# Performance work log

Hardware: AMD Instinct MI355X
Metric: run time of the kernel (lower is better)

## Reference

```python
import math
import jax, jax.numpy as jnp
import numpy as np

EMBED_DIM = 1024
N_HEADS = 16
HEAD_DIM = EMBED_DIM // N_HEADS
B, T = 4, 2048


def setup_inputs() -> dict:
    key = jax.random.key(0)
    k1, k2, k3 = jax.random.split(key, 3)
    scale_in = 1.0 / math.sqrt(EMBED_DIM)
    return {
        "x": jax.random.normal(k1, (B, T, EMBED_DIM), dtype=jnp.float32),
        "direction": 0,  # 0=FORWARD (causal), 1=RETRODICTION (anti-causal), 2=CORRECTION (causal)
        "qkv_w": jax.random.normal(k2, (EMBED_DIM, 3 * EMBED_DIM), dtype=jnp.float32) * scale_in,
        "qkv_b": jnp.zeros((3 * EMBED_DIM,), dtype=jnp.float32),
        "proj_w": jax.random.normal(k3, (EMBED_DIM, EMBED_DIM), dtype=jnp.float32) * scale_in,
        "proj_b": jnp.zeros((EMBED_DIM,), dtype=jnp.float32),
    }


def reference(x, direction, qkv_w, qkv_b, proj_w, proj_b):
    Bx, Tx, C = x.shape
    qkv = x @ qkv_w + qkv_b                        # [B,T,3C]
    q, k, v = jnp.split(qkv, 3, axis=-1)
    # [B,T,C] -> [B,H,T,D]
    def heads(t):
        return t.reshape(Bx, Tx, N_HEADS, HEAD_DIM).transpose(0, 2, 1, 3)
    q, k, v = heads(q), heads(k), heads(v)
    scale = 1.0 / math.sqrt(HEAD_DIM)
    attn = jnp.einsum('bhqd,bhkd->bhqk', q, k) * scale
    rows = jnp.arange(Tx)[:, None]
    cols = jnp.arange(Tx)[None, :]
    if direction == 1:  # RETRODICTION -> anti-causal (upper triangular allowed)
        mask = cols >= rows
    else:               # FORWARD / CORRECTION -> causal
        mask = cols <= rows
    attn = jnp.where(mask[None, None], attn, -jnp.inf)
    attn = jax.nn.softmax(attn, axis=-1)  # dropout p=0 -> identity
    out = jnp.einsum('bhqk,bhkd->bhqd', attn, v)   # [B,H,T,D]
    out = out.transpose(0, 2, 1, 3).reshape(Bx, Tx, C)
    return out @ proj_w + proj_b
```

## Files before the change

kernel.cpp:

```cpp
#include <hip/hip_runtime.h>
#include <math.h>

typedef __bf16 bf16_t;
typedef bf16_t bf16x8 __attribute__((ext_vector_type(8)));
typedef bf16_t bf16x4 __attribute__((ext_vector_type(4)));
typedef float  f32x4  __attribute__((ext_vector_type(4)));
typedef float  floatv4 __attribute__((ext_vector_type(4)));

#define AS1 __attribute__((address_space(1)))
#define AS3 __attribute__((address_space(3)))

static __device__ __forceinline__ void gld_lds16(const void* g, void* l) {
  __builtin_amdgcn_global_load_lds((const AS1 unsigned int*)g,
                                   (AS3 unsigned int*)l, 16, 0, 0);
}
static __device__ __forceinline__ void block_sync() {
  asm volatile("" ::: "memory");
  __builtin_amdgcn_s_barrier();
  asm volatile("" ::: "memory");
}

__global__ __launch_bounds__(256) void k_cast(const float* __restrict__ in,
                                              bf16_t* __restrict__ out, int n4) {
  int i = blockIdx.x * 256 + threadIdx.x;
  if (i >= n4) return;
  floatv4 v = ((const floatv4*)in)[i];
  bf16x4 o;
  o.x = (bf16_t)v.x; o.y = (bf16_t)v.y; o.z = (bf16_t)v.z; o.w = (bf16_t)v.w;
  ((bf16x4*)out)[i] = o;
}

__global__ __launch_bounds__(256) void k_transpose_cast(const float* __restrict__ in,
                                                        bf16_t* __restrict__ out,
                                                        int R, int Cc) {
  __shared__ float tile[32][33];
  int c0 = blockIdx.x * 32, r0 = blockIdx.y * 32;
  int tx = threadIdx.x, ty = threadIdx.y;
#pragma unroll
  for (int i = 0; i < 32; i += 8)
    tile[ty + i][tx] = in[(size_t)(r0 + ty + i) * Cc + c0 + tx];
  __syncthreads();
#pragma unroll
  for (int i = 0; i < 32; i += 8)
    out[(size_t)(c0 + ty + i) * R + r0 + tx] = (bf16_t)tile[tx][ty + i];
}

__global__ __launch_bounds__(512, 2) void k_gemm_qkv(
    const bf16_t* __restrict__ A, const bf16_t* __restrict__ Bt,
    const float* __restrict__ bias,
    bf16_t* __restrict__ qo, bf16_t* __restrict__ ko, bf16_t* __restrict__ vto) {
  const int K = 1024;
  __shared__ __align__(16) char smem[122880];
  const int m0 = blockIdx.x * 256, n0 = blockIdx.y * 384;
  const int t = threadIdx.x, lane = t & 63, wv = t >> 6;
  const int ln15 = lane & 15, lhi = lane >> 4;
  const int wr = wv >> 2, wc = wv & 3;

  f32x4 acc[8][6];
#pragma unroll
  for (int m = 0; m < 8; ++m)
#pragma unroll
    for (int n = 0; n < 6; ++n) acc[m][n] = (f32x4){0.f, 0.f, 0.f, 0.f};
  bf16x8 af[4], bfr[6];

  const bf16_t* aS = A + (size_t)(m0 + wv * 16 + ln15) * K + lhi * 8;
  const bf16_t* bS = Bt + (size_t)(n0 + wv * 16 + ln15) * K + lhi * 8;
  const int dA = wv * 1024 + lane * 16;

  auto stageA = [&](int k0, char* buf) {
    gld_lds16(aS + k0, buf + dA);
    gld_lds16(aS + (size_t)128 * K + k0, buf + 8192 + dA);
  };
  auto stageB = [&](int k0, char* buf) {
    gld_lds16(bS + k0, buf + 16384 + dA);
    gld_lds16(bS + (size_t)128 * K + k0, buf + 24576 + dA);
    gld_lds16(bS + (size_t)256 * K + k0, buf + 32768 + dA);
  };

  char* b0 = smem;
  char* b1 = smem + 40960;
  char* b2 = smem + 81920;
  stageA(0, b0); stageB(0, b0);
  stageA(32, b1); stageB(32, b1);
  asm volatile("s_waitcnt vmcnt(5)" ::: "memory");
  block_sync();

#pragma unroll 1
  for (int it = 0; it < 32; ++it) {
    const bool st = (it + 2 < 32);
    const int k0n = (it + 2) * 32;
#pragma unroll
    for (int m = 0; m < 4; ++m)
      af[m] = *(const bf16x8*)(b0 + (wr * 8 + m) * 1024 + lane * 16);
#pragma unroll
    for (int n = 0; n < 6; ++n)
      bfr[n] = *(const bf16x8*)(b0 + 16384 + (wc * 6 + n) * 1024 + lane * 16);
    if (st) stageA(k0n, b2);
    block_sync();
    asm volatile("s_waitcnt lgkmcnt(0)" ::: "memory");
    __builtin_amdgcn_sched_barrier(0);
    __builtin_amdgcn_s_setprio(1);
#pragma unroll
    for (int m = 0; m < 4; ++m)
#pragma unroll
      for (int n = 0; n < 6; ++n)
        acc[m][n] = __builtin_amdgcn_mfma_f32_16x16x32_bf16(af[m], bfr[n], acc[m][n], 0, 0, 0);
    __builtin_amdgcn_s_setprio(0);
    block_sync();
#pragma unroll
    for (int m = 0; m < 4; ++m)
      af[m] = *(const bf16x8*)(b0 + (wr * 8 + 4 + m) * 1024 + lane * 16);
    if (st) stageB(k0n, b2);
    block_sync();
    asm volatile("s_waitcnt lgkmcnt(0)" ::: "memory");
    __builtin_amdgcn_sched_barrier(0);
    __builtin_amdgcn_s_setprio(1);
#pragma unroll
    for (int m = 0; m < 4; ++m)
#pragma unroll
      for (int n = 0; n < 6; ++n)
        acc[4 + m][n] = __builtin_amdgcn_mfma_f32_16x16x32_bf16(af[m], bfr[n], acc[4 + m][n], 0, 0, 0);
    __builtin_amdgcn_s_setprio(0);
    if (st) asm volatile("s_waitcnt vmcnt(5)" ::: "memory");
    else if (it + 1 < 32) asm volatile("s_waitcnt vmcnt(0)" ::: "memory");
    block_sync();
    char* tmp = b0; b0 = b1; b1 = b2; b2 = tmp;
  }

  bf16_t* L = (bf16_t*)smem;
  const int bq = m0 >> 11, ttb = m0 & 2047;
#pragma unroll 1
  for (int p = 0; p < 3; ++p) {
    const int wcol0 = n0 + p * 128;
    const int which = wcol0 >> 10;
    const float bscale = (which == 0) ? 0.18033688011112042f : 1.0f;
#pragma unroll
    for (int n = 0; n < 6; ++n) {
      const int c16 = wc * 6 + n;
      if ((c16 >> 3) == p) {
        const int colL = c16 * 16 - p * 128 + ln15;
        const float bv = bias[n0 + c16 * 16 + ln15];
#pragma unroll
        for (int m = 0; m < 8; ++m)
#pragma unroll
          for (int j = 0; j < 4; ++j) {
            const int row = wr * 128 + m * 16 + lhi * 4 + j;
            const bf16_t ob = (bf16_t)((acc[m][n][j] + bv) * bscale);
            if (which == 2) L[colL * 264 + row] = ob;
            else            L[row * 132 + colL] = ob;
          }
      }
    }
    block_sync();
    if (which == 2) {
#pragma unroll
      for (int c = 0; c < 8; ++c) {
        const int idx = c * 512 + t;
        const int vcol = idx >> 5, r8 = (idx & 31) * 8;
        bf16x8 v8 = *(const bf16x8*)&L[vcol * 264 + r8];
        const int cc = (wcol0 & 1023) + vcol;
        const int hh = cc >> 6, d = cc & 63;
        *(bf16x8*)&vto[((size_t)(bq * 16 + hh) * 64 + d) * 2048 + ttb + r8] = v8;
      }
    } else {
      bf16_t* dst = (which == 0) ? qo : ko;
#pragma unroll
      for (int c = 0; c < 8; ++c) {
        const int idx = c * 512 + t;
        const int row = idx >> 4, c8 = (idx & 15) * 8;
        bf16x8 v8 = *(const bf16x8*)&L[row * 132 + c8];
        const int cc = (wcol0 & 1023) + c8;
        const int hh = cc >> 6, d = cc & 63;
        *(bf16x8*)&dst[((size_t)(bq * 16 + hh) * 2048 + ttb + row) * 64 + d] = v8;
      }
    }
    block_sync();
  }
}

__global__ __launch_bounds__(256) void k_attn3(
    const bf16_t* __restrict__ q, const bf16_t* __restrict__ k,
    const bf16_t* __restrict__ vt, const int* __restrict__ dirp,
    bf16_t* __restrict__ a2) {
  const int T = 2048;
  __shared__ __align__(16) bf16_t smem[16384];
  const int bh = blockIdx.x, b = bh >> 4, h = bh & 15;
  const int jb = blockIdx.y;
  const int t = threadIdx.x, lane = t & 63, w = t >> 6;
  const int ln15 = lane & 15, lhi = lane >> 4;
  const bool anti = (*dirp == 1);

  const bf16_t* kbase = k + (size_t)bh * T * 64;
  const bf16_t* vbase = vt + (size_t)bh * 64 * T;

  auto stage = [&](int kc0, int buf) {
    char* Kd = (char*)smem + buf * 16384;
    char* Vd = Kd + 8192;
#pragma unroll
    for (int s = 0; s < 2; ++s) {
      const int qk = s * 4 + (t >> 6);
      const int krow = kc0 + (qk >> 2) * 32 + ((qk >> 1) & 1) * 4 +
                       ((lane & 15) >> 2) * 8 + (lane & 3);
      const int kcolb = (lane >> 4) * 16 + (qk & 1) * 64;
      gld_lds16((const char*)kbase + (size_t)krow * 128 + kcolb,
                Kd + s * 4096 + t * 16);
      const int gv = qk;
      const int vd = (gv & 3) * 16 + (lane & 15);
      gld_lds16((const char*)vbase + (size_t)vd * 4096 + (size_t)kc0 * 2 +
                    (gv >> 2) * 64 + (lane >> 4) * 16,
                Vd + s * 4096 + t * 16);
    }
  };

#pragma unroll 1
  for (int sel = 0; sel < 2; ++sel) {
    const int qt = sel ? (31 - jb) : jb;
    const int q0 = qt * 64 + w * 16;
    const int qrow = q0 + ln15;

    const bf16_t* qp = q + ((size_t)bh * T + qrow) * 64 + lhi * 8;
    bf16x8 qf0 = *(const bf16x8*)qp;
    bf16x8 qf1 = *(const bf16x8*)(qp + 32);

    f32x4 acc[4];
#pragma unroll
    for (int g = 0; g < 4; ++g) acc[g] = (f32x4){0.f, 0.f, 0.f, 0.f};
    float mrun = -3.0e38f, lrun = 0.f;

    const int kt0 = anti ? qt : 0;
    const int nb = anti ? (32 - qt) : (qt + 1);

    stage(kt0 * 64, 0);
#pragma unroll 1
    for (int i = 0; i < nb; ++i) {
      const int kt = kt0 + i;
      const int buf = i & 1;
      if (i + 1 < nb) {
        stage((kt + 1) * 64, buf ^ 1);
        asm volatile("s_waitcnt vmcnt(4)" ::: "memory");
      } else {
        asm volatile("s_waitcnt vmcnt(0)" ::: "memory");
      }
      block_sync();
      const bf16_t* Kb = smem + buf * 8192;
      const bf16_t* Vb = Kb + 4096;

      float sc[16];
#pragma unroll
      for (int kh = 0; kh < 2; ++kh) {
        bf16x8 k0 = *(const bf16x8*)(Kb + (kh * 4 + 0) * 512 + lane * 8);
        bf16x8 k1 = *(const bf16x8*)(Kb + (kh * 4 + 1) * 512 + lane * 8);
        bf16x8 k2 = *(const bf16x8*)(Kb + (kh * 4 + 2) * 512 + lane * 8);
        bf16x8 k3 = *(const bf16x8*)(Kb + (kh * 4 + 3) * 512 + lane * 8);
        const f32x4 zz = (f32x4){0.f, 0.f, 0.f, 0.f};
        f32x4 slo = __builtin_amdgcn_mfma_f32_16x16x32_bf16(k0, qf0, zz, 0, 0, 0);
        slo = __builtin_amdgcn_mfma_f32_16x16x32_bf16(k1, qf1, slo, 0, 0, 0);
        f32x4 shi = __builtin_amdgcn_mfma_f32_16x16x32_bf16(k2, qf0, zz, 0, 0, 0);
        shi = __builtin_amdgcn_mfma_f32_16x16x32_bf16(k3, qf1, shi, 0, 0, 0);
#pragma unroll
        for (int j = 0; j < 4; ++j) {
          sc[kh * 8 + j] = slo[j];
          sc[kh * 8 + 4 + j] = shi[j];
        }
      }
      if (kt == qt) {
#pragma unroll
        for (int e = 0; e < 16; ++e) {
          const int col = kt * 64 + (e >> 3) * 32 + lhi * 8 + (e & 7);
          const bool ok = anti ? (col >= qrow) : (col <= qrow);
          sc[e] = ok ? sc[e] : -3.0e38f;
        }
      }
      float lmax = sc[0];
#pragma unroll
      for (int e = 1; e < 16; ++e) lmax = fmaxf(lmax, sc[e]);
      if (!__all(lmax <= mrun + 8.f)) {
        float vm = lmax;
        vm = fmaxf(vm, __shfl_xor(vm, 16));
        vm = fmaxf(vm, __shfl_xor(vm, 32));
        const float mn = fmaxf(mrun, vm);
        const float al = __builtin_amdgcn_exp2f(mrun - mn);
        lrun *= al;
#pragma unroll
        for (int g = 0; g < 4; ++g) acc[g] *= al;
        mrun = mn;
      }
      bf16x8 pb0, pb1;
      float rs = 0.f;
#pragma unroll
      for (int e = 0; e < 8; ++e) {
        float p = __builtin_amdgcn_exp2f(sc[e] - mrun);
        rs += p; pb0[e] = (bf16_t)p;
      }
#pragma unroll
      for (int e = 0; e < 8; ++e) {
        float p = __builtin_amdgcn_exp2f(sc[8 + e] - mrun);
        rs += p; pb1[e] = (bf16_t)p;
      }
      lrun += rs;
#pragma unroll
      for (int dg = 0; dg < 4; ++dg) {
        bf16x8 v0 = *(const bf16x8*)(Vb + dg * 512 + lane * 8);
        acc[dg] = __builtin_amdgcn_mfma_f32_16x16x32_bf16(v0, pb0, acc[dg], 0, 0, 0);
      }
#pragma unroll
      for (int dg = 0; dg < 4; ++dg) {
        bf16x8 v1 = *(const bf16x8*)(Vb + (4 + dg) * 512 + lane * 8);
        acc[dg] = __builtin_amdgcn_mfma_f32_16x16x32_bf16(v1, pb1, acc[dg], 0, 0, 0);
      }
      block_sync();
    }

    lrun += __shfl_xor(lrun, 16);
    lrun += __shfl_xor(lrun, 32);
    const float inv = __builtin_amdgcn_rcpf(lrun);
    bf16_t* op = a2 + ((size_t)b * T + qrow) * 1024 + h * 64 + lhi * 4;
#pragma unroll
    for (int g = 0; g < 4; ++g) {
      bf16x4 o4;
#pragma unroll
      for (int jx = 0; jx < 4; ++jx) o4[jx] = (bf16_t)(acc[g][jx] * inv);
      *(bf16x4*)(op + g * 16) = o4;
    }
  }
}

__global__ __launch_bounds__(512, 2) void k_gemm_proj(
    const bf16_t* __restrict__ A, const bf16_t* __restrict__ Bt,
    const float* __restrict__ bias, float* __restrict__ out) {
  const int K = 1024;
  __shared__ __align__(16) char smem[73728];
  const int m0 = blockIdx.x * 256, n0 = blockIdx.y * 128;
  const int t = threadIdx.x, lane = t & 63, wv = t >> 6;
  const int ln15 = lane & 15, lhi = lane >> 4;
  const int wr = wv >> 2, wc = wv & 3;

  f32x4 acc[8][2];
#pragma unroll
  for (int m = 0; m < 8; ++m)
#pragma unroll
    for (int n = 0; n < 2; ++n) acc[m][n] = (f32x4){0.f, 0.f, 0.f, 0.f};
  bf16x8 af[4], bfr[2];

  const bf16_t* aS = A + (size_t)(m0 + wv * 16 + ln15) * K + lhi * 8;
  const bf16_t* bS = Bt + (size_t)(n0 + wv * 16 + ln15) * K + lhi * 8;
  const int dA = wv * 1024 + lane * 16;

  auto stageA = [&](int k0, char* buf) {
    gld_lds16(aS + k0, buf + dA);
    gld_lds16(aS + (size_t)128 * K + k0, buf + 8192 + dA);
  };
  auto stageB = [&](int k0, char* buf) {
    gld_lds16(bS + k0, buf + 16384 + dA);
  };

  char* b0 = smem;
  char* b1 = smem + 24576;
  char* b2 = smem + 49152;
  stageA(0, b0); stageB(0, b0);
  stageA(32, b1); stageB(32, b1);
  asm volatile("s_waitcnt vmcnt(3)" ::: "memory");
  block_sync();

#pragma unroll 1
  for (int it = 0; it < 32; ++it) {
    const bool st = (it + 2 < 32);
    const int k0n = (it + 2) * 32;
#pragma unroll
    for (int m = 0; m < 4; ++m)
      af[m] = *(const bf16x8*)(b0 + (wr * 8 + m) * 1024 + lane * 16);
#pragma unroll
    for (int n = 0; n < 2; ++n)
      bfr[n] = *(const bf16x8*)(b0 + 16384 + (wc * 2 + n) * 1024 + lane * 16);
    if (st) stageA(k0n, b2);
    block_sync();
    asm volatile("s_waitcnt lgkmcnt(0)" ::: "memory");
    __builtin_amdgcn_sched_barrier(0);
    __builtin_amdgcn_s_setprio(1);
#pragma unroll
    for (int m = 0; m < 4; ++m)
#pragma unroll
      for (int n = 0; n < 2; ++n)
        acc[m][n] = __builtin_amdgcn_mfma_f32_16x16x32_bf16(af[m], bfr[n], acc[m][n], 0, 0, 0);
    __builtin_amdgcn_s_setprio(0);
    block_sync();
#pragma unroll
    for (int m = 0; m < 4; ++m)
      af[m] = *(const bf16x8*)(b0 + (wr * 8 + 4 + m) * 1024 + lane * 16);
    if (st) stageB(k0n, b2);
    block_sync();
    asm volatile("s_waitcnt lgkmcnt(0)" ::: "memory");
    __builtin_amdgcn_sched_barrier(0);
    __builtin_amdgcn_s_setprio(1);
#pragma unroll
    for (int m = 0; m < 4; ++m)
#pragma unroll
      for (int n = 0; n < 2; ++n)
        acc[4 + m][n] = __builtin_amdgcn_mfma_f32_16x16x32_bf16(af[m], bfr[n], acc[4 + m][n], 0, 0, 0);
    __builtin_amdgcn_s_setprio(0);
    if (st) asm volatile("s_waitcnt vmcnt(3)" ::: "memory");
    else if (it + 1 < 32) asm volatile("s_waitcnt vmcnt(0)" ::: "memory");
    block_sync();
    char* tmp = b0; b0 = b1; b1 = b2; b2 = tmp;
  }

#pragma unroll
  for (int n = 0; n < 2; ++n) {
    const int col = n0 + wc * 32 + n * 16 + ln15;
    const float bv = bias[col];
#pragma unroll
    for (int m = 0; m < 8; ++m)
#pragma unroll
      for (int j = 0; j < 4; ++j) {
        const int row = m0 + wr * 128 + m * 16 + lhi * 4 + j;
        out[(size_t)row * 1024 + col] = acc[m][n][j] + bv;
      }
  }
}

extern "C" void kernel_launch(void* const* d_in, const int* in_sizes, int n_in,
                              void* d_out, int out_size, void* d_ws, size_t ws_size,
                              hipStream_t stream) {
  (void)in_sizes; (void)n_in; (void)out_size; (void)ws_size;
  const float* x      = (const float*)d_in[0];
  const int*   dirp   = (const int*)d_in[1];
  const float* qkv_w  = (const float*)d_in[2];
  const float* qkv_b  = (const float*)d_in[3];
  const float* proj_w = (const float*)d_in[4];
  const float* proj_b = (const float*)d_in[5];
  float* out = (float*)d_out;

  char* ws = (char*)d_ws;
  bf16_t* xb   = (bf16_t*)(ws);
  bf16_t* wq_t = (bf16_t*)(ws + 16777216);
  bf16_t* wp_t = (bf16_t*)(ws + 23068672);
  bf16_t* qb   = (bf16_t*)(ws + 25165824);
  bf16_t* kb   = (bf16_t*)(ws + 41943040);
  bf16_t* vtb  = (bf16_t*)(ws + 58720256);
  bf16_t* a2   = xb;

  k_cast<<<8192, 256, 0, stream>>>(x, xb, 2097152);
  k_transpose_cast<<<dim3(96, 32), dim3(32, 8), 0, stream>>>(qkv_w, wq_t, 1024, 3072);
  k_transpose_cast<<<dim3(32, 32), dim3(32, 8), 0, stream>>>(proj_w, wp_t, 1024, 1024);
  k_gemm_qkv<<<dim3(32, 8), 512, 0, stream>>>(xb, wq_t, qkv_b, qb, kb, vtb);
  k_attn3<<<dim3(64, 16), 256, 0, stream>>>(qb, kb, vtb, dirp, a2);
  k_gemm_proj<<<dim3(32, 8), 512, 0, stream>>>(a2, wp_t, proj_b, out);
}
```

Before: 197.5 us.

## Enlarge attention query tile to 128 rows so each K/V stage feeds two query groups

```diff
diff --git a/kernel.cpp b/kernel.cpp
--- a/kernel.cpp
+++ b/kernel.cpp
@@ -178,7 +178,7 @@
   }
 }
 
-__global__ __launch_bounds__(256) void k_attn3(
+__global__ __launch_bounds__(256) void k_attn4(
     const bf16_t* __restrict__ q, const bf16_t* __restrict__ k,
     const bf16_t* __restrict__ vt, const int* __restrict__ dirp,
     bf16_t* __restrict__ a2) {
@@ -186,7 +186,7 @@
   __shared__ __align__(16) bf16_t smem[16384];
   const int bh = blockIdx.x, b = bh >> 4, h = bh & 15;
   const int jb = blockIdx.y;
-  const int t = threadIdx.x, lane = t & 63, w = t >> 6;
+  const int t = threadIdx.x, lane = t & 63, wv = t >> 6;
   const int ln15 = lane & 15, lhi = lane >> 4;
   const bool anti = (*dirp == 1);
 
@@ -198,37 +198,41 @@
     char* Vd = Kd + 8192;
 #pragma unroll
     for (int s = 0; s < 2; ++s) {
-      const int qk = s * 4 + (t >> 6);
+      const int qk = s * 4 + wv;
       const int krow = kc0 + (qk >> 2) * 32 + ((qk >> 1) & 1) * 4 +
                        ((lane & 15) >> 2) * 8 + (lane & 3);
       const int kcolb = (lane >> 4) * 16 + (qk & 1) * 64;
       gld_lds16((const char*)kbase + (size_t)krow * 128 + kcolb,
                 Kd + s * 4096 + t * 16);
-      const int gv = qk;
-      const int vd = (gv & 3) * 16 + (lane & 15);
+      const int vd = (qk & 3) * 16 + (lane & 15);
       gld_lds16((const char*)vbase + (size_t)vd * 4096 + (size_t)kc0 * 2 +
-                    (gv >> 2) * 64 + (lane >> 4) * 16,
+                    (qk >> 2) * 64 + (lane >> 4) * 16,
                 Vd + s * 4096 + t * 16);
     }
   };
 
 #pragma unroll 1
   for (int sel = 0; sel < 2; ++sel) {
-    const int qt = sel ? (31 - jb) : jb;
-    const int q0 = qt * 64 + w * 16;
-    const int qrow = q0 + ln15;
-
-    const bf16_t* qp = q + ((size_t)bh * T + qrow) * 64 + lhi * 8;
-    bf16x8 qf0 = *(const bf16x8*)qp;
-    bf16x8 qf1 = *(const bf16x8*)(qp + 32);
-
-    f32x4 acc[4];
-#pragma unroll
-    for (int g = 0; g < 4; ++g) acc[g] = (f32x4){0.f, 0.f, 0.f, 0.f};
-    float mrun = -3.0e38f, lrun = 0.f;
-
-    const int kt0 = anti ? qt : 0;
-    const int nb = anti ? (32 - qt) : (qt + 1);
+    const int qt = sel ? (15 - jb) : jb;
+    const int q0w = qt * 128 + wv * 32;
+
+    bf16x8 qf[2][2];
+#pragma unroll
+    for (int g = 0; g < 2; ++g) {
+      const bf16_t* qp = q + ((size_t)bh * T + q0w + g * 16 + ln15) * 64 + lhi * 8;
+      qf[g][0] = *(const bf16x8*)qp;
+      qf[g][1] = *(const bf16x8*)(qp + 32);
+    }
+
+    f32x4 acc[2][4];
+#pragma unroll
+    for (int g = 0; g < 2; ++g)
+#pragma unroll
+      for (int dg = 0; dg < 4; ++dg) acc[g][dg] = (f32x4){0.f, 0.f, 0.f, 0.f};
+    float mrun[2] = {-3.0e38f, -3.0e38f}, lrun[2] = {0.f, 0.f};
+
+    const int kt0 = anti ? 2 * qt : 0;
+    const int nb  = anti ? (32 - 2 * qt) : (2 * qt + 2);
 
     stage(kt0 * 64, 0);
 #pragma unroll 1
@@ -245,82 +249,98 @@
       const bf16_t* Kb = smem + buf * 8192;
       const bf16_t* Vb = Kb + 4096;
 
-      float sc[16];
-#pragma unroll
-      for (int kh = 0; kh < 2; ++kh) {
-        bf16x8 k0 = *(const bf16x8*)(Kb + (kh * 4 + 0) * 512 + lane * 8);
-        bf16x8 k1 = *(const bf16x8*)(Kb + (kh * 4 + 1) * 512 + lane * 8);
-        bf16x8 k2 = *(const bf16x8*)(Kb + (kh * 4 + 2) * 512 + lane * 8);
-        bf16x8 k3 = *(const bf16x8*)(Kb + (kh * 4 + 3) * 512 + lane * 8);
-        const f32x4 zz = (f32x4){0.f, 0.f, 0.f, 0.f};
-        f32x4 slo = __builtin_amdgcn_mfma_f32_16x16x32_bf16(k0, qf0, zz, 0, 0, 0);
-        slo = __builtin_amdgcn_mfma_f32_16x16x32_bf16(k1, qf1, slo, 0, 0, 0);
-        f32x4 shi = __builtin_amdgcn_mfma_f32_16x16x32_bf16(k2, qf0, zz, 0, 0, 0);
-        shi = __builtin_amdgcn_mfma_f32_16x16x32_bf16(k3, qf1, shi, 0, 0, 0);
-#pragma unroll
-        for (int j = 0; j < 4; ++j) {
-          sc[kh * 8 + j] = slo[j];
-          sc[kh * 8 + 4 + j] = shi[j];
+      const bool active = anti ? (kt * 64 + 63 >= q0w) : (kt * 64 <= q0w + 31);
+      if (active) {
+        float sc[2][16];
+#pragma unroll
+        for (int kh = 0; kh < 2; ++kh) {
+          bf16x8 kf0 = *(const bf16x8*)(Kb + (kh * 4 + 0) * 512 + lane * 8);
+          bf16x8 kf1 = *(const bf16x8*)(Kb + (kh * 4 + 1) * 512 + lane * 8);
+          bf16x8 kf2 = *(const bf16x8*)(Kb + (kh * 4 + 2) * 512 + lane * 8);
+          bf16x8 kf3 = *(const bf16x8*)(Kb + (kh * 4 + 3) * 512 + lane * 8);
+#pragma unroll
+          for (int g = 0; g < 2; ++g) {
+            const f32x4 zz = (f32x4){0.f, 0.f, 0.f, 0.f};
+            f32x4 slo = __builtin_amdgcn_mfma_f32_16x16x32_bf16(kf0, qf[g][0], zz, 0, 0, 0);
+            slo = __builtin_amdgcn_mfma_f32_16x16x32_bf16(kf1, qf[g][1], slo, 0, 0, 0);
+            f32x4 shi = __builtin_amdgcn_mfma_f32_16x16x32_bf16(kf2, qf[g][0], zz, 0, 0, 0);
+            shi = __builtin_amdgcn_mfma_f32_16x16x32_bf16(kf3, qf[g][1], shi, 0, 0, 0);
+#pragma unroll
+            for (int j = 0; j < 4; ++j) {
+              sc[g][kh * 8 + j] = slo[j];
+              sc[g][kh * 8 + 4 + j] = shi[j];
+            }
+          }
         }
-      }
-      if (kt == qt) {
-#pragma unroll
-        for (int e = 0; e < 16; ++e) {
-          const int col = kt * 64 + (e >> 3) * 32 + lhi * 8 + (e & 7);
-          const bool ok = anti ? (col >= qrow) : (col <= qrow);
-          sc[e] = ok ? sc[e] : -3.0e38f;
+        bf16x8 vfr[8];
+#pragma unroll
+        for (int dg = 0; dg < 8; ++dg)
+          vfr[dg] = *(const bf16x8*)(Vb + dg * 512 + lane * 8);
+#pragma unroll
+        for (int g = 0; g < 2; ++g) {
+          const int grow = q0w + g * 16 + ln15;
+          const bool needm = anti ? (kt * 64 < q0w + g * 16 + 15)
+                                  : (kt * 64 + 63 > q0w + g * 16);
+          if (needm) {
+#pragma unroll
+            for (int e = 0; e < 16; ++e) {
+              const int col = kt * 64 + (e >> 3) * 32 + lhi * 8 + (e & 7);
+              const bool ok = anti ? (col >= grow) : (col <= grow);
+              sc[g][e] = ok ? sc[g][e] : -3.0e38f;
+            }
+          }
+          float lmax = sc[g][0];
+#pragma unroll
+          for (int e = 1; e < 16; ++e) lmax = fmaxf(lmax, sc[g][e]);
+          if (!__all(lmax <= mrun[g] + 8.f)) {
+            float vm = lmax;
+            vm = fmaxf(vm, __shfl_xor(vm, 16));
+            vm = fmaxf(vm, __shfl_xor(vm, 32));
+            const float mn = fmaxf(mrun[g], vm);
+            const float al = __builtin_amdgcn_exp2f(mrun[g] - mn);
+            lrun[g] *= al;
+#pragma unroll
+            for (int dg = 0; dg < 4; ++dg) acc[g][dg] *= al;
+            mrun[g] = mn;
+          }
+          bf16x8 pb0, pb1;
+          float rs = 0.f;
+#pragma unroll
+          for (int e = 0; e < 8; ++e) {
+            float p = __builtin_amdgcn_exp2f(sc[g][e] - mrun[g]);
+            rs += p; pb0[e] = (bf16_t)p;
+          }
+#pragma unroll
+          for (int e = 0; e < 8; ++e) {
+            float p = __builtin_amdgcn_exp2f(sc[g][8 + e] - mrun[g]);
+            rs += p; pb1[e] = (bf16_t)p;
+          }
+          lrun[g] += rs;
+#pragma unroll
+          for (int dg = 0; dg < 4; ++dg)
+            acc[g][dg] = __builtin_amdgcn_mfma_f32_16x16x32_bf16(vfr[dg], pb0, acc[g][dg], 0, 0, 0);
+#pragma unroll
+          for (int dg = 0; dg < 4; ++dg)
+            acc[g][dg] = __builtin_amdgcn_mfma_f32_16x16x32_bf16(vfr[4 + dg], pb1, acc[g][dg], 0, 0, 0);
         }
       }
-      float lmax = sc[0];
-#pragma unroll
-      for (int e = 1; e < 16; ++e) lmax = fmaxf(lmax, sc[e]);
-      if (!__all(lmax <= mrun + 8.f)) {
-        float vm = lmax;
-        vm = fmaxf(vm, __shfl_xor(vm, 16));
-        vm = fmaxf(vm, __shfl_xor(vm, 32));
-        const float mn = fmaxf(mrun, vm);
-        const float al = __builtin_amdgcn_exp2f(mrun - mn);
-        lrun *= al;
-#pragma unroll
-        for (int g = 0; g < 4; ++g) acc[g] *= al;
-        mrun = mn;
-      }
-      bf16x8 pb0, pb1;
-      float rs = 0.f;
-#pragma unroll
-      for (int e = 0; e < 8; ++e) {
-        float p = __builtin_amdgcn_exp2f(sc[e] - mrun);
-        rs += p; pb0[e] = (bf16_t)p;
-      }
-#pragma unroll
-      for (int e = 0; e < 8; ++e) {
-        float p = __builtin_amdgcn_exp2f(sc[8 + e] - mrun);
-        rs += p; pb1[e] = (bf16_t)p;
-      }
-      lrun += rs;
+      block_sync();
+    }
+
+#pragma unroll
+    for (int g = 0; g < 2; ++g) {
+      float l = lrun[g];
+      l += __shfl_xor(l, 16);
+      l += __shfl_xor(l, 32);
+      const float inv = __builtin_amdgcn_rcpf(l);
+      bf16_t* op = a2 + ((size_t)b * T + q0w + g * 16 + ln15) * 1024 + h * 64 + lhi * 4;
 #pragma unroll
       for (int dg = 0; dg < 4; ++dg) {
-        bf16x8 v0 = *(const bf16x8*)(Vb + dg * 512 + lane * 8);
-        acc[dg] = __builtin_amdgcn_mfma_f32_16x16x32_bf16(v0, pb0, acc[dg], 0, 0, 0);
-      }
-#pragma unroll
-      for (int dg = 0; dg < 4; ++dg) {
-        bf16x8 v1 = *(const bf16x8*)(Vb + (4 + dg) * 512 + lane * 8);
-        acc[dg] = __builtin_amdgcn_mfma_f32_16x16x32_bf16(v1, pb1, acc[dg], 0, 0, 0);
-      }
-      block_sync();
-    }
-
-    lrun += __shfl_xor(lrun, 16);
-    lrun += __shfl_xor(lrun, 32);
-    const float inv = __builtin_amdgcn_rcpf(lrun);
-    bf16_t* op = a2 + ((size_t)b * T + qrow) * 1024 + h * 64 + lhi * 4;
-#pragma unroll
-    for (int g = 0; g < 4; ++g) {
-      bf16x4 o4;
-#pragma unroll
-      for (int jx = 0; jx < 4; ++jx) o4[jx] = (bf16_t)(acc[g][jx] * inv);
-      *(bf16x4*)(op + g * 16) = o4;
+        bf16x4 o4;
+#pragma unroll
+        for (int jx = 0; jx < 4; ++jx) o4[jx] = (bf16_t)(acc[g][dg][jx] * inv);
+        *(bf16x4*)(op + dg * 16) = o4;
+      }
     }
   }
 }
@@ -443,6 +463,6 @@
   k_transpose_cast<<<dim3(96, 32), dim3(32, 8), 0, stream>>>(qkv_w, wq_t, 1024, 3072);
   k_transpose_cast<<<dim3(32, 32), dim3(32, 8), 0, stream>>>(proj_w, wp_t, 1024, 1024);
   k_gemm_qkv<<<dim3(32, 8), 512, 0, stream>>>(xb, wq_t, qkv_b, qb, kb, vtb);
-  k_attn3<<<dim3(64, 16), 256, 0, stream>>>(qb, kb, vtb, dirp, a2);
+  k_attn4<<<dim3(64, 8), 256, 0, stream>>>(qb, kb, vtb, dirp, a2);
   k_gemm_proj<<<dim3(32, 8), 512, 0, stream>>>(a2, wp_t, proj_b, out);
 }
```

Result: faster. 193.1 us (-2.2%).
